# Optimization experiments

Hardware: AMD Instinct MI355X
Metric: run time of the kernel (lower is better)

The kernel has to match this reference:

```python
import jax, jax.numpy as jnp
import numpy as np

HIDDEN, FFN, N_EXPERTS, TOP_K = 1024, 4096, 8, 2


def setup_inputs() -> dict:
    key = jax.random.key(0)
    ks = jax.random.split(key, 8)
    s_h = 1.0 / np.sqrt(HIDDEN)
    s_f = 1.0 / np.sqrt(FFN)
    return {
        "x": jax.random.normal(ks[0], (1, 1024, HIDDEN), dtype=jnp.float32),
        "gate_w": jax.random.normal(ks[1], (N_EXPERTS, HIDDEN), dtype=jnp.float32) * s_h,
        "gate_b": jnp.zeros((N_EXPERTS,), dtype=jnp.float32),
        "w1": jax.random.normal(ks[2], (N_EXPERTS, HIDDEN, FFN), dtype=jnp.float32) * s_h,
        "b1": jnp.zeros((N_EXPERTS, FFN), dtype=jnp.float32),
        "w2": jax.random.normal(ks[3], (N_EXPERTS, FFN, HIDDEN), dtype=jnp.float32) * s_f,
        "b2": jnp.zeros((N_EXPERTS, HIDDEN), dtype=jnp.float32),
    }


def reference(x, gate_w, gate_b, w1, b1, w2, b2):
    B, S, H = x.shape
    x_flat = x.reshape(-1, H)  # (T, H)
    # Router: top-k gating with softmax over selected logits
    logits = x_flat @ gate_w.T + gate_b  # (T, E)
    top_w, sel = jax.lax.top_k(logits, TOP_K)  # (T, K)
    rw = jax.nn.softmax(top_w, axis=-1)  # (T, K)
    # combine[t, e] = router weight of expert e for token t (0 if not selected)
    combine = jnp.sum(jax.nn.one_hot(sel, N_EXPERTS, dtype=x.dtype) * rw[..., None], axis=1)  # (T, E)
    # Dense all-expert FFN, combined with routing weights (zero weight => zero contribution,
    # identical math to the masked gather/scatter loop in the torch module)
    h = jax.nn.gelu(jnp.einsum('th,ehf->tef', x_flat, w1) + b1, approximate=False)  # (T, E, F)
    y = jnp.einsum('tef,efh->teh', h, w2) + b2  # (T, E, H)
    out = jnp.einsum('te,teh->th', combine, y)  # (T, H)
    return out.reshape(B, S, H)
```

## Files before the change

### kernel.cpp

```cpp
#include <hip/hip_runtime.h>


typedef __bf16 bf16;
typedef __bf16 bf16x8 __attribute__((ext_vector_type(8)));
typedef float floatx4 __attribute__((ext_vector_type(4)));

#define T_TOK 1024
#define HID 1024
#define FFN 4096
#define NEXP 8
#define BM 128
#define BN 128
#define BK 32
#define LP 36

__global__ void xconv_k(const float* __restrict__ x, bf16* __restrict__ xb) {
  int i = blockIdx.x * 256 + threadIdx.x;
  float4 a = ((const float4*)x)[i * 2];
  float4 b = ((const float4*)x)[i * 2 + 1];
  bf16 t[8] = {(bf16)a.x, (bf16)a.y, (bf16)a.z, (bf16)a.w,
               (bf16)b.x, (bf16)b.y, (bf16)b.z, (bf16)b.w};
  *(bf16x8*)&xb[(size_t)i * 8] = *(bf16x8*)t;
}

__global__ void router_k(const float* __restrict__ x, const float* __restrict__ gw,
                         const float* __restrict__ gb, int* __restrict__ cnt,
                         int* __restrict__ elist, float* __restrict__ ewt) {
  int wave = threadIdx.x >> 6;
  int lane = threadIdx.x & 63;
  int t = blockIdx.x * 4 + wave;
  const float* xr = x + (size_t)t * HID;
  float xv[16];
#pragma unroll
  for (int j = 0; j < 16; j++) xv[j] = xr[lane + 64 * j];
  float logits[NEXP];
#pragma unroll
  for (int e = 0; e < NEXP; e++) {
    const float* g = gw + (size_t)e * HID;
    float s = 0.f;
#pragma unroll
    for (int j = 0; j < 16; j++) s += xv[j] * g[lane + 64 * j];
#pragma unroll
    for (int off = 32; off; off >>= 1) s += __shfl_xor(s, off, 64);
    logits[e] = s + gb[e];
  }
  int i0 = 0; float l0 = logits[0];
#pragma unroll
  for (int e = 1; e < NEXP; e++) if (logits[e] > l0) { l0 = logits[e]; i0 = e; }
  int i1 = -1; float l1 = -3.0e38f;
#pragma unroll
  for (int e = 0; e < NEXP; e++) if (e != i0 && logits[e] > l1) { l1 = logits[e]; i1 = e; }
  if (lane == 0) {
    float w0 = 1.f / (1.f + expf(l1 - l0));
    float w1 = 1.f - w0;
    int p0 = atomicAdd(cnt + i0, 1);
    elist[i0 * T_TOK + p0] = t * 2 + 0; ewt[i0 * T_TOK + p0] = w0;
    int p1 = atomicAdd(cnt + i1, 1);
    elist[i1 * T_TOK + p1] = t * 2 + 1; ewt[i1 * T_TOK + p1] = w1;
  }
}

__global__ __launch_bounds__(256)
void gemm1_k(const bf16* __restrict__ xb, const float* __restrict__ w1,
             const float* __restrict__ b1, const int* __restrict__ cnt,
             const int* __restrict__ elist, bf16* __restrict__ hbuf) {
  int e = blockIdx.z;
  int c = cnt[e];
  int m0 = blockIdx.y * BM;
  if (m0 >= c) return;
  int n0 = blockIdx.x * BN;

  __shared__ __align__(16) bf16 As[BM][LP];
  __shared__ __align__(16) bf16 Bs[BN][LP];

  int tid = threadIdx.x;
  int ar = tid >> 1;
  int ac = (tid & 1) * 16;
  int ra = m0 + ar; if (ra >= c) ra = c - 1;
  const bf16* aptr = xb + (size_t)(elist[e * T_TOK + ra] >> 1) * HID + ac;
  int bn = tid & 127;
  int bk = (tid >> 7) * 16;
  const float* bptr = w1 + (size_t)e * HID * FFN + (size_t)bk * FFN + n0 + bn;

  uint4 a0, a1;
  float bfl[16];
  a0 = *(const uint4*)(aptr);
  a1 = *(const uint4*)(aptr + 8);
#pragma unroll
  for (int j = 0; j < 16; j++) bfl[j] = bptr[(size_t)j * FFN];

  floatx4 acc[4][4] = {};
  int ln = tid & 63, wv = tid >> 6;
  int fm = ln & 15, quad = ln >> 4;
  int wm = (wv & 1) * 64, wn = (wv >> 1) * 64;

  for (int t = 0; t < HID / BK; t++) {
    bf16 bb[16];
#pragma unroll
    for (int j = 0; j < 16; j++) bb[j] = (bf16)bfl[j];
    uint4 wa0 = a0, wa1 = a1;
    __syncthreads();
    *(uint4*)&As[ar][ac]      = wa0;
    *(uint4*)&As[ar][ac + 8]  = wa1;
    *(bf16x8*)&Bs[bn][bk]     = *(bf16x8*)&bb[0];
    *(bf16x8*)&Bs[bn][bk + 8] = *(bf16x8*)&bb[8];
    if (t + 1 < HID / BK) {
      aptr += BK;
      a0 = *(const uint4*)(aptr);
      a1 = *(const uint4*)(aptr + 8);
      bptr += (size_t)BK * FFN;
#pragma unroll
      for (int j = 0; j < 16; j++) bfl[j] = bptr[(size_t)j * FFN];
    }
    __syncthreads();
    bf16x8 af[4], bfr[4];
#pragma unroll
    for (int i = 0; i < 4; i++) af[i] = *(const bf16x8*)&As[wm + i * 16 + fm][quad * 8];
#pragma unroll
    for (int j = 0; j < 4; j++) bfr[j] = *(const bf16x8*)&Bs[wn + j * 16 + fm][quad * 8];
#pragma unroll
    for (int i = 0; i < 4; i++)
#pragma unroll
      for (int j = 0; j < 4; j++)
        acc[i][j] = __builtin_amdgcn_mfma_f32_16x16x32_bf16(af[i], bfr[j], acc[i][j], 0, 0, 0);
  }

  const float* b1e = b1 + (size_t)e * FFN;
#pragma unroll
  for (int i = 0; i < 4; i++) {
    int rb = m0 + wm + i * 16 + quad * 4;
#pragma unroll
    for (int j = 0; j < 4; j++) {
      int col = n0 + wn + j * 16 + fm;
      float bias = b1e[col];
#pragma unroll
      for (int r = 0; r < 4; r++) {
        int row = rb + r;
        if (row < c) {
          int slot = elist[e * T_TOK + row];
          float v = acc[i][j][r] + bias;
          float g = 0.5f * v * (1.f + erff(v * 0.70710678118654752f));
          hbuf[(size_t)slot * FFN + col] = (bf16)g;
        }
      }
    }
  }
}

__global__ __launch_bounds__(256)
void gemm2_k(const bf16* __restrict__ hbuf, const float* __restrict__ w2,
             const float* __restrict__ b2, const int* __restrict__ cnt,
             const int* __restrict__ elist, const float* __restrict__ ewt,
             float* __restrict__ part) {
  int e = blockIdx.z & 7;
  int ks = blockIdx.z >> 3;
  int c = cnt[e];
  int m0 = blockIdx.y * BM;
  if (m0 >= c) return;
  int n0 = blockIdx.x * BN;
  int kbeg = ks * (FFN / 4);

  __shared__ __align__(16) bf16 As[BM][LP];
  __shared__ __align__(16) bf16 Bs[BN][LP];

  int tid = threadIdx.x;
  int ar = tid >> 1;
  int ac = (tid & 1) * 16;
  int ra = m0 + ar; if (ra >= c) ra = c - 1;
  const bf16* aptr = hbuf + (size_t)elist[e * T_TOK + ra] * FFN + kbeg + ac;
  int bn = tid & 127;
  int bk = (tid >> 7) * 16;
  const float* bptr = w2 + (size_t)e * FFN * HID + (size_t)(kbeg + bk) * HID + n0 + bn;

  uint4 a0, a1;
  float bfl[16];
  a0 = *(const uint4*)(aptr);
  a1 = *(const uint4*)(aptr + 8);
#pragma unroll
  for (int j = 0; j < 16; j++) bfl[j] = bptr[(size_t)j * HID];

  floatx4 acc[4][4] = {};
  int ln = tid & 63, wv = tid >> 6;
  int fm = ln & 15, quad = ln >> 4;
  int wm = (wv & 1) * 64, wn = (wv >> 1) * 64;

  const int NT = (FFN / 4) / BK;
  for (int t = 0; t < NT; t++) {
    bf16 bb[16];
#pragma unroll
    for (int j = 0; j < 16; j++) bb[j] = (bf16)bfl[j];
    uint4 wa0 = a0, wa1 = a1;
    __syncthreads();
    *(uint4*)&As[ar][ac]      = wa0;
    *(uint4*)&As[ar][ac + 8]  = wa1;
    *(bf16x8*)&Bs[bn][bk]     = *(bf16x8*)&bb[0];
    *(bf16x8*)&Bs[bn][bk + 8] = *(bf16x8*)&bb[8];
    if (t + 1 < NT) {
      aptr += BK;
      a0 = *(const uint4*)(aptr);
      a1 = *(const uint4*)(aptr + 8);
      bptr += (size_t)BK * HID;
#pragma unroll
      for (int j = 0; j < 16; j++) bfl[j] = bptr[(size_t)j * HID];
    }
    __syncthreads();
    bf16x8 af[4], bfr[4];
#pragma unroll
    for (int i = 0; i < 4; i++) af[i] = *(const bf16x8*)&As[wm + i * 16 + fm][quad * 8];
#pragma unroll
    for (int j = 0; j < 4; j++) bfr[j] = *(const bf16x8*)&Bs[wn + j * 16 + fm][quad * 8];
#pragma unroll
    for (int i = 0; i < 4; i++)
#pragma unroll
      for (int j = 0; j < 4; j++)
        acc[i][j] = __builtin_amdgcn_mfma_f32_16x16x32_bf16(af[i], bfr[j], acc[i][j], 0, 0, 0);
  }

  const float* b2e = b2 + (size_t)e * HID;
#pragma unroll
  for (int i = 0; i < 4; i++) {
    int rb = m0 + wm + i * 16 + quad * 4;
#pragma unroll
    for (int j = 0; j < 4; j++) {
      int col = n0 + wn + j * 16 + fm;
      float bias = (ks == 0) ? b2e[col] : 0.f;
#pragma unroll
      for (int r = 0; r < 4; r++) {
        int row = rb + r;
        if (row < c) {
          int slot = elist[e * T_TOK + row];
          float w = ewt[e * T_TOK + row];
          part[((size_t)ks * (2 * T_TOK) + slot) * HID + col] = w * (acc[i][j][r] + bias);
        }
      }
    }
  }
}

__global__ void combine_k(const float* __restrict__ part, float* __restrict__ out) {
  int i = blockIdx.x * 256 + threadIdx.x;
  int t = i >> 8;
  int h4 = (i & 255) * 4;
  float4 s = {0.f, 0.f, 0.f, 0.f};
#pragma unroll
  for (int ks = 0; ks < 4; ks++)
#pragma unroll
    for (int sl = 0; sl < 2; sl++) {
      float4 v = *(const float4*)&part[((size_t)ks * (2 * T_TOK) + t * 2 + sl) * HID + h4];
      s.x += v.x; s.y += v.y; s.z += v.z; s.w += v.w;
    }
  *(float4*)&out[(size_t)t * HID + h4] = s;
}

extern "C" void kernel_launch(void* const* d_in, const int* in_sizes, int n_in,
                              void* d_out, int out_size, void* d_ws, size_t ws_size,
                              hipStream_t stream) {
  const float* x  = (const float*)d_in[0];
  const float* gw = (const float*)d_in[1];
  const float* gb = (const float*)d_in[2];
  const float* w1 = (const float*)d_in[3];
  const float* b1 = (const float*)d_in[4];
  const float* w2 = (const float*)d_in[5];
  const float* b2 = (const float*)d_in[6];
  float* out = (float*)d_out;

  char* ws = (char*)d_ws;
  int*   cnt   = (int*)ws;
  int*   elist = (int*)(ws + 1024);
  float* ewt   = (float*)(ws + 1024 + 32768);
  bf16*  xb    = (bf16*)(ws + (1 << 16));
  bf16*  hbuf  = (bf16*)(ws + ((size_t)4 << 20));
  float* part  = (float*)(ws + ((size_t)24 << 20));

  hipMemsetAsync(cnt, 0, 32, stream);
  xconv_k<<<512, 256, 0, stream>>>(x, xb);
  router_k<<<T_TOK / 4, 256, 0, stream>>>(x, gw, gb, cnt, elist, ewt);
  gemm1_k<<<dim3(FFN / BN, 8, NEXP), 256, 0, stream>>>(xb, w1, b1, cnt, elist, hbuf);
  gemm2_k<<<dim3(HID / BN, 8, NEXP * 4), 256, 0, stream>>>(hbuf, w2, b2, cnt, elist, ewt, part);
  combine_k<<<(T_TOK * HID / 4) / 256, 256, 0, stream>>>(part, out);
}
```

Baseline: 436.5 us.

## Pre-convert expert weights to transposed bf16 before each GEMM

```diff
diff --git a/kernel.cpp b/kernel.cpp
--- a/kernel.cpp
+++ b/kernel.cpp
@@ -23,6 +23,26 @@
   *(bf16x8*)&xb[(size_t)i * 8] = *(bf16x8*)t;
 }
 
+__global__ void wconv_k(const float* __restrict__ w, bf16* __restrict__ wt,
+                        int K, int N, int lgN, int lgKC) {
+  int gid = blockIdx.x * 256 + threadIdx.x;
+  int n = gid & (N - 1);
+  int kc = (gid >> lgN) & ((K >> 5) - 1);
+  int e = gid >> (lgN + lgKC);
+  const float* src = w + ((size_t)e * K + (size_t)kc * 32) * N + n;
+  bf16* dst = wt + ((size_t)e * N + n) * (size_t)K + kc * 32;
+  float v[32];
+#pragma unroll
+  for (int j = 0; j < 32; j++) v[j] = src[(size_t)j * N];
+  bf16x8 pk[4];
+#pragma unroll
+  for (int q = 0; q < 4; q++)
+#pragma unroll
+    for (int i = 0; i < 8; i++) pk[q][i] = (bf16)v[q * 8 + i];
+#pragma unroll
+  for (int q = 0; q < 4; q++) *(bf16x8*)(dst + q * 8) = pk[q];
+}
+
 __global__ void router_k(const float* __restrict__ x, const float* __restrict__ gw,
                          const float* __restrict__ gb, int* __restrict__ cnt,
                          int* __restrict__ elist, float* __restrict__ ewt) {
@@ -61,7 +81,7 @@
 }
 
 __global__ __launch_bounds__(256)
-void gemm1_k(const bf16* __restrict__ xb, const float* __restrict__ w1,
+void gemm1_k(const bf16* __restrict__ xb, const bf16* __restrict__ w1t,
              const float* __restrict__ b1, const int* __restrict__ cnt,
              const int* __restrict__ elist, bf16* __restrict__ hbuf) {
   int e = blockIdx.z;
@@ -78,16 +98,13 @@
   int ac = (tid & 1) * 16;
   int ra = m0 + ar; if (ra >= c) ra = c - 1;
   const bf16* aptr = xb + (size_t)(elist[e * T_TOK + ra] >> 1) * HID + ac;
-  int bn = tid & 127;
-  int bk = (tid >> 7) * 16;
-  const float* bptr = w1 + (size_t)e * HID * FFN + (size_t)bk * FFN + n0 + bn;
-
-  uint4 a0, a1;
-  float bfl[16];
+  const bf16* bptr = w1t + (size_t)e * FFN * HID + (size_t)(n0 + ar) * HID + ac;
+
+  uint4 a0, a1, b0, b1r;
   a0 = *(const uint4*)(aptr);
   a1 = *(const uint4*)(aptr + 8);
-#pragma unroll
-  for (int j = 0; j < 16; j++) bfl[j] = bptr[(size_t)j * FFN];
+  b0 = *(const uint4*)(bptr);
+  b1r = *(const uint4*)(bptr + 8);
 
   floatx4 acc[4][4] = {};
   int ln = tid & 63, wv = tid >> 6;
@@ -95,22 +112,19 @@
   int wm = (wv & 1) * 64, wn = (wv >> 1) * 64;
 
   for (int t = 0; t < HID / BK; t++) {
-    bf16 bb[16];
-#pragma unroll
-    for (int j = 0; j < 16; j++) bb[j] = (bf16)bfl[j];
-    uint4 wa0 = a0, wa1 = a1;
-    __syncthreads();
-    *(uint4*)&As[ar][ac]      = wa0;
-    *(uint4*)&As[ar][ac + 8]  = wa1;
-    *(bf16x8*)&Bs[bn][bk]     = *(bf16x8*)&bb[0];
-    *(bf16x8*)&Bs[bn][bk + 8] = *(bf16x8*)&bb[8];
+    uint4 wa0 = a0, wa1 = a1, wb0 = b0, wb1 = b1r;
+    __syncthreads();
+    *(uint4*)&As[ar][ac]     = wa0;
+    *(uint4*)&As[ar][ac + 8] = wa1;
+    *(uint4*)&Bs[ar][ac]     = wb0;
+    *(uint4*)&Bs[ar][ac + 8] = wb1;
     if (t + 1 < HID / BK) {
       aptr += BK;
+      bptr += BK;
       a0 = *(const uint4*)(aptr);
       a1 = *(const uint4*)(aptr + 8);
-      bptr += (size_t)BK * FFN;
-#pragma unroll
-      for (int j = 0; j < 16; j++) bfl[j] = bptr[(size_t)j * FFN];
+      b0 = *(const uint4*)(bptr);
+      b1r = *(const uint4*)(bptr + 8);
     }
     __syncthreads();
     bf16x8 af[4], bfr[4];
@@ -148,7 +162,7 @@
 }
 
 __global__ __launch_bounds__(256)
-void gemm2_k(const bf16* __restrict__ hbuf, const float* __restrict__ w2,
+void gemm2_k(const bf16* __restrict__ hbuf, const bf16* __restrict__ w2t,
              const float* __restrict__ b2, const int* __restrict__ cnt,
              const int* __restrict__ elist, const float* __restrict__ ewt,
              float* __restrict__ part) {
@@ -168,16 +182,13 @@
   int ac = (tid & 1) * 16;
   int ra = m0 + ar; if (ra >= c) ra = c - 1;
   const bf16* aptr = hbuf + (size_t)elist[e * T_TOK + ra] * FFN + kbeg + ac;
-  int bn = tid & 127;
-  int bk = (tid >> 7) * 16;
-  const float* bptr = w2 + (size_t)e * FFN * HID + (size_t)(kbeg + bk) * HID + n0 + bn;
-
-  uint4 a0, a1;
-  float bfl[16];
+  const bf16* bptr = w2t + (size_t)e * HID * FFN + (size_t)(n0 + ar) * FFN + kbeg + ac;
+
+  uint4 a0, a1, b0, b1r;
   a0 = *(const uint4*)(aptr);
   a1 = *(const uint4*)(aptr + 8);
-#pragma unroll
-  for (int j = 0; j < 16; j++) bfl[j] = bptr[(size_t)j * HID];
+  b0 = *(const uint4*)(bptr);
+  b1r = *(const uint4*)(bptr + 8);
 
   floatx4 acc[4][4] = {};
   int ln = tid & 63, wv = tid >> 6;
@@ -186,22 +197,19 @@
 
   const int NT = (FFN / 4) / BK;
   for (int t = 0; t < NT; t++) {
-    bf16 bb[16];
-#pragma unroll
-    for (int j = 0; j < 16; j++) bb[j] = (bf16)bfl[j];
-    uint4 wa0 = a0, wa1 = a1;
-    __syncthreads();
-    *(uint4*)&As[ar][ac]      = wa0;
-    *(uint4*)&As[ar][ac + 8]  = wa1;
-    *(bf16x8*)&Bs[bn][bk]     = *(bf16x8*)&bb[0];
-    *(bf16x8*)&Bs[bn][bk + 8] = *(bf16x8*)&bb[8];
+    uint4 wa0 = a0, wa1 = a1, wb0 = b0, wb1 = b1r;
+    __syncthreads();
+    *(uint4*)&As[ar][ac]     = wa0;
+    *(uint4*)&As[ar][ac + 8] = wa1;
+    *(uint4*)&Bs[ar][ac]     = wb0;
+    *(uint4*)&Bs[ar][ac + 8] = wb1;
     if (t + 1 < NT) {
       aptr += BK;
+      bptr += BK;
       a0 = *(const uint4*)(aptr);
       a1 = *(const uint4*)(aptr + 8);
-      bptr += (size_t)BK * HID;
-#pragma unroll
-      for (int j = 0; j < 16; j++) bfl[j] = bptr[(size_t)j * HID];
+      b0 = *(const uint4*)(bptr);
+      b1r = *(const uint4*)(bptr + 8);
     }
     __syncthreads();
     bf16x8 af[4], bfr[4];
@@ -270,12 +278,15 @@
   float* ewt   = (float*)(ws + 1024 + 32768);
   bf16*  xb    = (bf16*)(ws + (1 << 16));
   bf16*  hbuf  = (bf16*)(ws + ((size_t)4 << 20));
-  float* part  = (float*)(ws + ((size_t)24 << 20));
+  float* part  = (float*)(ws + ((size_t)21 << 20));
+  bf16*  wT    = (bf16*)(ws + ((size_t)55 << 20));
 
   hipMemsetAsync(cnt, 0, 32, stream);
   xconv_k<<<512, 256, 0, stream>>>(x, xb);
   router_k<<<T_TOK / 4, 256, 0, stream>>>(x, gw, gb, cnt, elist, ewt);
-  gemm1_k<<<dim3(FFN / BN, 8, NEXP), 256, 0, stream>>>(xb, w1, b1, cnt, elist, hbuf);
-  gemm2_k<<<dim3(HID / BN, 8, NEXP * 4), 256, 0, stream>>>(hbuf, w2, b2, cnt, elist, ewt, part);
+  wconv_k<<<4096, 256, 0, stream>>>(w1, wT, HID, FFN, 12, 5);
+  gemm1_k<<<dim3(FFN / BN, 8, NEXP), 256, 0, stream>>>(xb, wT, b1, cnt, elist, hbuf);
+  wconv_k<<<4096, 256, 0, stream>>>(w2, wT, FFN, HID, 10, 7);
+  gemm2_k<<<dim3(HID / BN, 8, NEXP * 4), 256, 0, stream>>>(hbuf, wT, b2, cnt, elist, ewt, part);
   combine_k<<<(T_TOK * HID / 4) / 256, 256, 0, stream>>>(part, out);
 }
```

Result: slower. 481.8 us (+10.4%).
